# Kernel tuning notes

Hardware: AMD Instinct MI355X
Metric: run time of the kernel (lower is better)

The kernel has to match this reference:

```python
import jax, jax.numpy as jnp
import numpy as np

LN_EPS = 1e-5

def setup_inputs() -> dict:
    key = jax.random.key(0)
    k0, k1, k2, k3 = jax.random.split(key, 4)
    B, N, D = 4, 4096, 512
    x = jax.random.normal(k0, (B, N, D), dtype=jnp.float32)
    s = 1.0 / np.sqrt(D)
    Wq = jax.random.normal(k1, (D, D), dtype=jnp.float32) * s
    Wk = jax.random.normal(k2, (D, D), dtype=jnp.float32) * s
    Wv = jax.random.normal(k3, (D, D), dtype=jnp.float32) * s
    gamma = jnp.ones((D,), dtype=jnp.float32)
    beta = jnp.zeros((D,), dtype=jnp.float32)
    return {"x": x, "Wq": Wq, "Wk": Wk, "Wv": Wv, "gamma": gamma, "beta": beta}

def reference(x, Wq, Wk, Wv, gamma, beta):
    # x: [B, N, D]
    D = x.shape[-1]
    q = jnp.einsum('bnd,de->bne', x, Wq)
    k = jnp.einsum('bnd,de->bne', x, Wk)
    v = jnp.einsum('bnd,de->bne', x, Wv)
    # full [B, N, N] score matrix, as in the original bmm chain
    dist = jnp.einsum('bne,bme->bnm', q, k) * (1.0 / jnp.sqrt(jnp.float32(D)))
    dist = jax.nn.softmax(dist, axis=-1)
    att = jnp.einsum('bnm,bmd->bnd', dist, v)
    # residual + LayerNorm over last dim
    h = att + x
    mu = jnp.mean(h, axis=-1, keepdims=True)
    var = jnp.mean(jnp.square(h - mu), axis=-1, keepdims=True)
    out = (h - mu) * jax.lax.rsqrt(var + LN_EPS) * gamma + beta
    return out
```

## Files before the change

### kernel.cpp

```cpp
#include <hip/hip_runtime.h>
#include <stdint.h>

typedef __attribute__((ext_vector_type(8))) __bf16 bf16x8;
typedef __attribute__((ext_vector_type(4))) float f32x4;
typedef __attribute__((ext_vector_type(16))) float f32x16;
typedef unsigned short u16;
typedef unsigned int u32;

#define LN_EPS 1e-5f

__device__ __forceinline__ float bf2f(u16 u){
  union { u32 i; float f; } v; v.i = ((u32)u) << 16; return v.f;
}
__device__ __forceinline__ u16 f2bf(float f){
  union { float f; u32 i; } v; v.f = f;
  u32 u = v.i;
  u += 0x7fffu + ((u >> 16) & 1u);
  return (u16)(u >> 16);
}

__device__ __forceinline__ void gload_lds16(const u16* g, u16* l) {
  __builtin_amdgcn_global_load_lds(
      (const __attribute__((address_space(1))) void*)g,
      (__attribute__((address_space(3))) void*)l, 16, 0, 0);
}

__global__ void transpose_w_kernel(const float* __restrict__ Wq,
                                   const float* __restrict__ Wk,
                                   const float* __restrict__ Wv,
                                   u16* __restrict__ Wt) {
  const float* W = (blockIdx.y == 0) ? Wq : ((blockIdx.y == 1) ? Wk : Wv);
  u16* o = Wt + blockIdx.y * 512 * 512;
  int idx = blockIdx.x * 256 + threadIdx.x;
  int e = idx >> 9, d = idx & 511;
  o[e * 512 + d] = f2bf(W[d * 512 + e]);
}

__launch_bounds__(256, 2)
__global__ void qkv_gemm_kernel(const float* __restrict__ X,
                                const u16* __restrict__ Wt,
                                u16* __restrict__ Qo,
                                u16* __restrict__ Ko,
                                u16* __restrict__ Vto) {
  const int z = blockIdx.y;
  const u16* Wtm = Wt + z * 512 * 512;
  const int mblk = blockIdx.x & 127;
  const int nblk = blockIdx.x >> 7;
  const int m0 = mblk * 128, n0 = nblk * 128;

  __shared__ u16 As[128 * 40];
  __shared__ u16 Bs[128 * 40];

  const int tid = threadIdx.x;
  const int lane = tid & 63, w = tid >> 6;
  const int wr = w >> 1, wc = w & 1;
  const int lrow = lane & 15, quad = lane >> 4;

  f32x4 acc[4][4];
#pragma unroll
  for (int i = 0; i < 4; i++)
#pragma unroll
    for (int j = 0; j < 4; j++) acc[i][j] = (f32x4){0.f, 0.f, 0.f, 0.f};

  for (int k0 = 0; k0 < 512; k0 += 32) {
    __syncthreads();
#pragma unroll
    for (int i = 0; i < 2; i++) {
      int c = tid + i * 256;
      int r = c >> 2, cc = (c & 3) * 8;
      float4 f0 = *(const float4*)&X[(m0 + r) * 512 + k0 + cc];
      float4 f1 = *(const float4*)&X[(m0 + r) * 512 + k0 + cc + 4];
      ushort4 lo, hi;
      lo.x = f2bf(f0.x); lo.y = f2bf(f0.y); lo.z = f2bf(f0.z); lo.w = f2bf(f0.w);
      hi.x = f2bf(f1.x); hi.y = f2bf(f1.y); hi.z = f2bf(f1.z); hi.w = f2bf(f1.w);
      *(ushort4*)&As[r * 40 + cc] = lo;
      *(ushort4*)&As[r * 40 + cc + 4] = hi;
      uint4 vb = *(const uint4*)&Wtm[(n0 + r) * 512 + k0 + cc];
      *(uint4*)&Bs[r * 40 + cc] = vb;
    }
    __syncthreads();
    bf16x8 a[4], b[4];
#pragma unroll
    for (int t = 0; t < 4; t++)
      a[t] = *(const bf16x8*)&As[(wr * 64 + t * 16 + lrow) * 40 + quad * 8];
#pragma unroll
    for (int t = 0; t < 4; t++)
      b[t] = *(const bf16x8*)&Bs[(wc * 64 + t * 16 + lrow) * 40 + quad * 8];
#pragma unroll
    for (int i = 0; i < 4; i++)
#pragma unroll
      for (int j = 0; j < 4; j++)
        acc[i][j] = __builtin_amdgcn_mfma_f32_16x16x32_bf16(a[i], b[j], acc[i][j], 0, 0, 0);
  }

  if (z < 2) {
    u16* O = (z == 0) ? Qo : Ko;
#pragma unroll
    for (int i = 0; i < 4; i++) {
      int rbase = m0 + wr * 64 + i * 16 + quad * 4;
#pragma unroll
      for (int j = 0; j < 4; j++) {
        int col = n0 + wc * 64 + j * 16 + lrow;
#pragma unroll
        for (int r = 0; r < 4; r++)
          O[(rbase + r) * 512 + col] = f2bf(acc[i][j][r]);
      }
    }
  } else {
#pragma unroll
    for (int i = 0; i < 4; i++) {
      int rbase = m0 + wr * 64 + i * 16 + quad * 4;
#pragma unroll
      for (int j = 0; j < 4; j++) {
        int col = n0 + wc * 64 + j * 16 + lrow;
        ushort4 pk;
        pk.x = f2bf(acc[i][j][0]);
        pk.y = f2bf(acc[i][j][1]);
        pk.z = f2bf(acc[i][j][2]);
        pk.w = f2bf(acc[i][j][3]);
        *(ushort4*)&Vto[col * 16384 + rbase] = pk;
      }
    }
  }
}

__launch_bounds__(256, 2)
__global__ void attn_partial_kernel(const u16* __restrict__ Q,
                                    const u16* __restrict__ K,
                                    const u16* __restrict__ Vt,
                                    float* __restrict__ O0,
                                    u16* __restrict__ O1,
                                    float* __restrict__ L) {
  const int b = blockIdx.y;
  const int split = blockIdx.z;
  const int q0 = blockIdx.x * 64;
  const int tid = threadIdx.x;
  const int lane = tid & 63, w = tid >> 6;
  const int lrow = lane & 15, quad = lane >> 4;
  const int l31 = lane & 31, half = lane >> 5;

  __shared__ u16 Ks[32 * 512];
  __shared__ u16 Vs[512 * 32];
  __shared__ u16 Pbuf[64 * 40];

  const int keybase = b * 4096 + split * 2048;

  const int qtok = b * 4096 + q0 + w * 16 + lrow;
  bf16x8 qf[16];
#pragma unroll
  for (int s = 0; s < 16; s++)
    qf[s] = *(const bf16x8*)&Q[qtok * 512 + s * 32 + quad * 8];

  f32x16 Oacc[2][4];
#pragma unroll
  for (int i = 0; i < 2; i++)
#pragma unroll
    for (int j = 0; j < 4; j++)
#pragma unroll
      for (int e = 0; e < 16; e++) Oacc[i][j][e] = 0.f;

  float lsum[4] = {0.f, 0.f, 0.f, 0.f};
  const float scale = 0.044194173824159216f;

#pragma unroll
  for (int i = 0; i < 8; i++) {
    int row = w * 8 + i;
    int c = lane ^ (row & 7);
    gload_lds16(&K[(keybase + row) * 512 + c * 8], &Ks[row * 512]);
  }
#pragma unroll
  for (int run = 0; run < 8; run++) {
    int rr = w * 8 + run;
    int n = rr * 16 + (lane >> 2);
    int c = (lane & 3) ^ (n & 3) ^ ((n >> 2) & 3);
    gload_lds16(&Vt[n * 16384 + keybase + c * 8], &Vs[rr * 512]);
  }

  for (int it = 0; it < 64; ++it) {
    __syncthreads();

    f32x4 S0 = {0.f, 0.f, 0.f, 0.f}, S1 = {0.f, 0.f, 0.f, 0.f};
#pragma unroll
    for (int s = 0; s < 16; s++) {
      int c0 = (s * 4 + quad) ^ (lrow & 7);
      bf16x8 k0f = *(const bf16x8*)&Ks[lrow * 512 + c0 * 8];
      bf16x8 k1f = *(const bf16x8*)&Ks[(16 + lrow) * 512 + c0 * 8];
      S0 = __builtin_amdgcn_mfma_f32_16x16x32_bf16(qf[s], k0f, S0, 0, 0, 0);
      S1 = __builtin_amdgcn_mfma_f32_16x16x32_bf16(qf[s], k1f, S1, 0, 0, 0);
    }

#pragma unroll
    for (int r = 0; r < 4; r++) {
      float p0 = __expf(S0[r] * scale);
      float p1 = __expf(S1[r] * scale);
      lsum[r] += p0 + p1;
      int prow = w * 16 + quad * 4 + r;
      Pbuf[prow * 40 + lrow] = f2bf(p0);
      Pbuf[prow * 40 + 16 + lrow] = f2bf(p1);
    }

    __syncthreads();

    const int kknext = (it + 1) * 32;
    if (it < 63) {
#pragma unroll
      for (int i = 0; i < 8; i++) {
        int row = w * 8 + i;
        int c = lane ^ (row & 7);
        gload_lds16(&K[(keybase + kknext + row) * 512 + c * 8], &Ks[row * 512]);
      }
    }

    bf16x8 af[2][2];
#pragma unroll
    for (int i = 0; i < 2; i++)
#pragma unroll
      for (int kg = 0; kg < 2; kg++)
        af[i][kg] = *(const bf16x8*)&Pbuf[(i * 32 + l31) * 40 + kg * 16 + half * 8];

#pragma unroll
    for (int j = 0; j < 4; j++) {
      bf16x8 bf_[2];
#pragma unroll
      for (int kg = 0; kg < 2; kg++) {
        int n = w * 128 + j * 32 + l31;
        int c = (kg * 2 + half) ^ (n & 3) ^ ((n >> 2) & 3);
        bf_[kg] = *(const bf16x8*)&Vs[n * 32 + c * 8];
      }
      if (it < 63) {
#pragma unroll
        for (int t = 0; t < 2; t++) {
          int rr = w * 8 + j * 2 + t;
          int n = rr * 16 + (lane >> 2);
          int c = (lane & 3) ^ (n & 3) ^ ((n >> 2) & 3);
          gload_lds16(&Vt[n * 16384 + keybase + kknext + c * 8], &Vs[rr * 512]);
        }
      }
#pragma unroll
      for (int i = 0; i < 2; i++) {
        Oacc[i][j] = __builtin_amdgcn_mfma_f32_32x32x16_bf16(af[i][0], bf_[0], Oacc[i][j], 0, 0, 0);
        Oacc[i][j] = __builtin_amdgcn_mfma_f32_32x32x16_bf16(af[i][1], bf_[1], Oacc[i][j], 0, 0, 0);
      }
    }
  }

#pragma unroll
  for (int r = 0; r < 4; r++) {
    float s = lsum[r];
    s += __shfl_xor(s, 1); s += __shfl_xor(s, 2);
    s += __shfl_xor(s, 4); s += __shfl_xor(s, 8);
    lsum[r] = s;
  }
  const int tokw = b * 4096 + q0 + w * 16 + quad * 4;
  if (lrow == 0) {
#pragma unroll
    for (int r = 0; r < 4; r++)
      L[split * 16384 + tokw + r] = lsum[r];
  }

  const int tokbase = b * 4096 + q0;
  if (split == 0) {
#pragma unroll
    for (int i = 0; i < 2; i++)
#pragma unroll
      for (int j = 0; j < 4; j++) {
        int col = w * 128 + j * 32 + l31;
#pragma unroll
        for (int p = 0; p < 16; p++) {
          int row = i * 32 + (p & 3) + 8 * (p >> 2) + 4 * half;
          O0[(tokbase + row) * 512 + col] = Oacc[i][j][p];
        }
      }
  } else {
#pragma unroll
    for (int i = 0; i < 2; i++)
#pragma unroll
      for (int j = 0; j < 4; j++) {
        int col = w * 128 + j * 32 + l31;
#pragma unroll
        for (int p = 0; p < 16; p++) {
          int row = i * 32 + (p & 3) + 8 * (p >> 2) + 4 * half;
          O1[(tokbase + row) * 512 + col] = f2bf(Oacc[i][j][p]);
        }
      }
  }
}

__launch_bounds__(256)
__global__ void combine_ln_kernel(const float* __restrict__ O0in,
                                  const u16* __restrict__ O1,
                                  const float* __restrict__ L,
                                  const float* __restrict__ X,
                                  const float* __restrict__ gamma,
                                  const float* __restrict__ beta,
                                  float* __restrict__ Out) {
  const int lane = threadIdx.x & 63;
  const int tok = blockIdx.x * 4 + (threadIdx.x >> 6);
  const float inv_l = 1.f / (L[tok] + L[16384 + tok]);
  const int base = tok * 512 + lane * 8;

  float4 a0 = *(const float4*)&O0in[base];
  float4 a1 = *(const float4*)&O0in[base + 4];
  uint4 bvec = *(const uint4*)&O1[base];
  const u16* bp = (const u16*)&bvec;
  float4 x0 = *(const float4*)&X[base];
  float4 x1 = *(const float4*)&X[base + 4];

  float h[8];
  h[0] = (a0.x + bf2f(bp[0])) * inv_l + x0.x;
  h[1] = (a0.y + bf2f(bp[1])) * inv_l + x0.y;
  h[2] = (a0.z + bf2f(bp[2])) * inv_l + x0.z;
  h[3] = (a0.w + bf2f(bp[3])) * inv_l + x0.w;
  h[4] = (a1.x + bf2f(bp[4])) * inv_l + x1.x;
  h[5] = (a1.y + bf2f(bp[5])) * inv_l + x1.y;
  h[6] = (a1.z + bf2f(bp[6])) * inv_l + x1.z;
  h[7] = (a1.w + bf2f(bp[7])) * inv_l + x1.w;

  float sum = 0.f, sq = 0.f;
#pragma unroll
  for (int i = 0; i < 8; i++) { sum += h[i]; sq += h[i] * h[i]; }
#pragma unroll
  for (int d = 1; d < 64; d <<= 1) {
    sum += __shfl_xor(sum, d);
    sq  += __shfl_xor(sq, d);
  }
  float mu = sum * (1.f / 512.f);
  float var = sq * (1.f / 512.f) - mu * mu;
  float rstd = rsqrtf(var + LN_EPS);

  float4 g0 = *(const float4*)&gamma[lane * 8];
  float4 g1 = *(const float4*)&gamma[lane * 8 + 4];
  float4 b0 = *(const float4*)&beta[lane * 8];
  float4 b1 = *(const float4*)&beta[lane * 8 + 4];

  float4 o0, o1;
  o0.x = (h[0] - mu) * rstd * g0.x + b0.x;
  o0.y = (h[1] - mu) * rstd * g0.y + b0.y;
  o0.z = (h[2] - mu) * rstd * g0.z + b0.z;
  o0.w = (h[3] - mu) * rstd * g0.w + b0.w;
  o1.x = (h[4] - mu) * rstd * g1.x + b1.x;
  o1.y = (h[5] - mu) * rstd * g1.y + b1.y;
  o1.z = (h[6] - mu) * rstd * g1.z + b1.z;
  o1.w = (h[7] - mu) * rstd * g1.w + b1.w;
  *(float4*)&Out[base] = o0;
  *(float4*)&Out[base + 4] = o1;
}

extern "C" void kernel_launch(void* const* d_in, const int* in_sizes, int n_in,
                              void* d_out, int out_size, void* d_ws, size_t ws_size,
                              hipStream_t stream) {
  const float* x = (const float*)d_in[0];
  const float* Wq = (const float*)d_in[1];
  const float* Wk = (const float*)d_in[2];
  const float* Wv = (const float*)d_in[3];
  const float* gamma = (const float*)d_in[4];
  const float* beta = (const float*)d_in[5];

  char* ws = (char*)d_ws;
  u16* Qws   = (u16*)(ws);
  u16* Kws   = (u16*)(ws + 16777216);
  u16* Vtws  = (u16*)(ws + 33554432);
  u16* Wtws  = (u16*)(ws + 50331648);
  u16* O1ws  = (u16*)(ws + 51904512);
  float* Lws = (float*)(ws + 68681728);
  float* O0  = (float*)d_out;

  hipLaunchKernelGGL(transpose_w_kernel, dim3(1024, 3), dim3(256), 0, stream,
                     Wq, Wk, Wv, Wtws);
  hipLaunchKernelGGL(qkv_gemm_kernel, dim3(512, 3), dim3(256), 0, stream,
                     x, Wtws, Qws, Kws, Vtws);
  hipLaunchKernelGGL(attn_partial_kernel, dim3(64, 4, 2), dim3(256), 0, stream,
                     Qws, Kws, Vtws, O0, O1ws, Lws);
  hipLaunchKernelGGL(combine_ln_kernel, dim3(4096), dim3(256), 0, stream,
                     O0, O1ws, Lws, x, gamma, beta, (float*)d_out);
}
```

Baseline: 330.2 us.

## Store Q/K as FP8 and use FP8 MFMA for attention scores

Q and K are now quantized to FP8 (e4m3) in the QKV GEMM epilogue, and the QK^T score computation uses the fp8 16x16x32 MFMA with 8-byte operands. This halves Q/K memory traffic and the K tile's LDS footprint, with a new swizzled K load layout. The V-tile prefetch is also restructured: all V fragments are read into registers first, then the next V tile is issued in one batch before the PV MFMAs. The cost is reduced precision in the attention scores, which may hurt accuracy.

```diff
diff --git a/kernel.cpp b/kernel.cpp
--- a/kernel.cpp
+++ b/kernel.cpp
@@ -5,7 +5,9 @@
 typedef __attribute__((ext_vector_type(4))) float f32x4;
 typedef __attribute__((ext_vector_type(16))) float f32x16;
 typedef unsigned short u16;
+typedef unsigned char u8;
 typedef unsigned int u32;
+typedef long i64;
 
 #define LN_EPS 1e-5f
 
@@ -18,8 +20,19 @@
   u += 0x7fffu + ((u >> 16) & 1u);
   return (u16)(u >> 16);
 }
-
-__device__ __forceinline__ void gload_lds16(const u16* g, u16* l) {
+__device__ __forceinline__ u8 f2fp8(float f){
+  union { float f; u32 i; } v; v.f = f;
+  u32 s = (v.i >> 24) & 0x80u;
+  u32 u = v.i & 0x7FFFFFFFu;
+  if (u < 0x3C800000u) return (u8)s;
+  if (u > 0x43E00000u) u = 0x43E00000u;
+  u += 0x7FFFFu + ((u >> 20) & 1u);
+  int e = (int)(u >> 23) - 120;
+  u32 m = (u >> 20) & 7u;
+  return (u8)(s | ((u32)e << 3) | m);
+}
+
+__device__ __forceinline__ void gload_lds16(const void* g, void* l) {
   __builtin_amdgcn_global_load_lds(
       (const __attribute__((address_space(1))) void*)g,
       (__attribute__((address_space(3))) void*)l, 16, 0, 0);
@@ -39,8 +52,8 @@
 __launch_bounds__(256, 2)
 __global__ void qkv_gemm_kernel(const float* __restrict__ X,
                                 const u16* __restrict__ Wt,
-                                u16* __restrict__ Qo,
-                                u16* __restrict__ Ko,
+                                u8* __restrict__ Qo,
+                                u8* __restrict__ Ko,
                                 u16* __restrict__ Vto) {
   const int z = blockIdx.y;
   const u16* Wtm = Wt + z * 512 * 512;
@@ -94,7 +107,7 @@
   }
 
   if (z < 2) {
-    u16* O = (z == 0) ? Qo : Ko;
+    u8* O = (z == 0) ? Qo : Ko;
 #pragma unroll
     for (int i = 0; i < 4; i++) {
       int rbase = m0 + wr * 64 + i * 16 + quad * 4;
@@ -103,7 +116,7 @@
         int col = n0 + wc * 64 + j * 16 + lrow;
 #pragma unroll
         for (int r = 0; r < 4; r++)
-          O[(rbase + r) * 512 + col] = f2bf(acc[i][j][r]);
+          O[(rbase + r) * 512 + col] = f2fp8(acc[i][j][r]);
       }
     }
   } else {
@@ -125,8 +138,8 @@
 }
 
 __launch_bounds__(256, 2)
-__global__ void attn_partial_kernel(const u16* __restrict__ Q,
-                                    const u16* __restrict__ K,
+__global__ void attn_partial_kernel(const u8* __restrict__ Q,
+                                    const u8* __restrict__ K,
                                     const u16* __restrict__ Vt,
                                     float* __restrict__ O0,
                                     u16* __restrict__ O1,
@@ -139,17 +152,17 @@
   const int lrow = lane & 15, quad = lane >> 4;
   const int l31 = lane & 31, half = lane >> 5;
 
-  __shared__ u16 Ks[32 * 512];
+  __shared__ __align__(16) u8 Ks8[32 * 512];
   __shared__ u16 Vs[512 * 32];
   __shared__ u16 Pbuf[64 * 40];
 
   const int keybase = b * 4096 + split * 2048;
 
   const int qtok = b * 4096 + q0 + w * 16 + lrow;
-  bf16x8 qf[16];
+  i64 qf[16];
 #pragma unroll
   for (int s = 0; s < 16; s++)
-    qf[s] = *(const bf16x8*)&Q[qtok * 512 + s * 32 + quad * 8];
+    qf[s] = *(const i64*)&Q[qtok * 512 + s * 32 + quad * 8];
 
   f32x16 Oacc[2][4];
 #pragma unroll
@@ -163,10 +176,10 @@
   const float scale = 0.044194173824159216f;
 
 #pragma unroll
-  for (int i = 0; i < 8; i++) {
-    int row = w * 8 + i;
-    int c = lane ^ (row & 7);
-    gload_lds16(&K[(keybase + row) * 512 + c * 8], &Ks[row * 512]);
+  for (int i = 0; i < 4; i++) {
+    int row = w * 8 + i * 2 + (lane >> 5);
+    int g = (lane & 31) ^ (row & 7);
+    gload_lds16(&K[(keybase + row) * 512 + g * 16], &Ks8[(w * 8 + i * 2) * 512]);
   }
 #pragma unroll
   for (int run = 0; run < 8; run++) {
@@ -182,11 +195,12 @@
     f32x4 S0 = {0.f, 0.f, 0.f, 0.f}, S1 = {0.f, 0.f, 0.f, 0.f};
 #pragma unroll
     for (int s = 0; s < 16; s++) {
-      int c0 = (s * 4 + quad) ^ (lrow & 7);
-      bf16x8 k0f = *(const bf16x8*)&Ks[lrow * 512 + c0 * 8];
-      bf16x8 k1f = *(const bf16x8*)&Ks[(16 + lrow) * 512 + c0 * 8];
-      S0 = __builtin_amdgcn_mfma_f32_16x16x32_bf16(qf[s], k0f, S0, 0, 0, 0);
-      S1 = __builtin_amdgcn_mfma_f32_16x16x32_bf16(qf[s], k1f, S1, 0, 0, 0);
+      int gs = (2 * s + (quad >> 1)) ^ (lrow & 7);
+      int off = gs * 16 + (quad & 1) * 8;
+      i64 k0 = *(const i64*)&Ks8[lrow * 512 + off];
+      i64 k1 = *(const i64*)&Ks8[(16 + lrow) * 512 + off];
+      S0 = __builtin_amdgcn_mfma_f32_16x16x32_fp8_fp8(qf[s], k0, S0, 0, 0, 0);
+      S1 = __builtin_amdgcn_mfma_f32_16x16x32_fp8_fp8(qf[s], k1, S1, 0, 0, 0);
     }
 
 #pragma unroll
@@ -204,10 +218,11 @@
     const int kknext = (it + 1) * 32;
     if (it < 63) {
 #pragma unroll
-      for (int i = 0; i < 8; i++) {
-        int row = w * 8 + i;
-        int c = lane ^ (row & 7);
-        gload_lds16(&K[(keybase + kknext + row) * 512 + c * 8], &Ks[row * 512]);
+      for (int i = 0; i < 4; i++) {
+        int row = w * 8 + i * 2 + (lane >> 5);
+        int g = (lane & 31) ^ (row & 7);
+        gload_lds16(&K[(keybase + kknext + row) * 512 + g * 16],
+                    &Ks8[(w * 8 + i * 2) * 512]);
       }
     }
 
@@ -218,30 +233,35 @@
       for (int kg = 0; kg < 2; kg++)
         af[i][kg] = *(const bf16x8*)&Pbuf[(i * 32 + l31) * 40 + kg * 16 + half * 8];
 
-#pragma unroll
-    for (int j = 0; j < 4; j++) {
-      bf16x8 bf_[2];
+    bf16x8 bv[4][2];
+#pragma unroll
+    for (int j = 0; j < 4; j++)
 #pragma unroll
       for (int kg = 0; kg < 2; kg++) {
         int n = w * 128 + j * 32 + l31;
         int c = (kg * 2 + half) ^ (n & 3) ^ ((n >> 2) & 3);
-        bf_[kg] = *(const bf16x8*)&Vs[n * 32 + c * 8];
-      }
-      if (it < 63) {
-#pragma unroll
-        for (int t = 0; t < 2; t++) {
-          int rr = w * 8 + j * 2 + t;
-          int n = rr * 16 + (lane >> 2);
-          int c = (lane & 3) ^ (n & 3) ^ ((n >> 2) & 3);
-          gload_lds16(&Vt[n * 16384 + keybase + kknext + c * 8], &Vs[rr * 512]);
-        }
-      }
+        bv[j][kg] = *(const bf16x8*)&Vs[n * 32 + c * 8];
+      }
+
+    asm volatile("s_waitcnt lgkmcnt(0)" ::: "memory");
+
+    if (it < 63) {
+#pragma unroll
+      for (int run = 0; run < 8; run++) {
+        int rr = w * 8 + run;
+        int n = rr * 16 + (lane >> 2);
+        int c = (lane & 3) ^ (n & 3) ^ ((n >> 2) & 3);
+        gload_lds16(&Vt[n * 16384 + keybase + kknext + c * 8], &Vs[rr * 512]);
+      }
+    }
+
+#pragma unroll
+    for (int j = 0; j < 4; j++)
 #pragma unroll
       for (int i = 0; i < 2; i++) {
-        Oacc[i][j] = __builtin_amdgcn_mfma_f32_32x32x16_bf16(af[i][0], bf_[0], Oacc[i][j], 0, 0, 0);
-        Oacc[i][j] = __builtin_amdgcn_mfma_f32_32x32x16_bf16(af[i][1], bf_[1], Oacc[i][j], 0, 0, 0);
-      }
-    }
+        Oacc[i][j] = __builtin_amdgcn_mfma_f32_32x32x16_bf16(af[i][0], bv[j][0], Oacc[i][j], 0, 0, 0);
+        Oacc[i][j] = __builtin_amdgcn_mfma_f32_32x32x16_bf16(af[i][1], bv[j][1], Oacc[i][j], 0, 0, 0);
+      }
   }
 
 #pragma unroll
@@ -357,12 +377,12 @@
   const float* beta = (const float*)d_in[5];
 
   char* ws = (char*)d_ws;
-  u16* Qws   = (u16*)(ws);
-  u16* Kws   = (u16*)(ws + 16777216);
-  u16* Vtws  = (u16*)(ws + 33554432);
-  u16* Wtws  = (u16*)(ws + 50331648);
-  u16* O1ws  = (u16*)(ws + 51904512);
-  float* Lws = (float*)(ws + 68681728);
+  u8*  Qws   = (u8*)(ws);
+  u8*  Kws   = (u8*)(ws + 8388608);
+  u16* Vtws  = (u16*)(ws + 16777216);
+  u16* Wtws  = (u16*)(ws + 33554432);
+  u16* O1ws  = (u16*)(ws + 35127296);
+  float* Lws = (float*)(ws + 51904512);
   float* O0  = (float*)d_out;
 
   hipLaunchKernelGGL(transpose_w_kernel, dim3(1024, 3), dim3(256), 0, stream,
```

Measured after the change: 290.8 us. -11.9%, faster.
